# Optimization experiments

Measured on AMD Instinct MI355X. Metric: run time of the kernel, lower is better.

Reference implementation:

```python
import jax, jax.numpy as jnp
import numpy as np

N, D, NC, K = 4096, 64, 1000, 8192
ALPHA, BETA, GAMMA, SUPT = 0.02, 1.0, 1.0, 1.0
TEMP, BASE_TEMP = 0.05, 0.05
L_INTRA, L_IMEAN, L_IMIN, L_FISHER, EPS = 1.0, 0.1, 0.05, 0.1, 1e-6


def _l2norm(x, axis):
    # torch F.normalize: x / max(||x||, 1e-12)
    n = jnp.sqrt(jnp.sum(x * x, axis=axis, keepdims=True))
    return x / jnp.maximum(n, 1e-12)


def setup_inputs() -> dict:
    key = jax.random.key(0)
    k1, k2, k3, k4, k5 = jax.random.split(key, 5)
    # long-tailed class counts -> log_prior and class_weight buffers
    cls_arr = np.maximum((1280.0 * 0.01 ** (np.arange(NC) / (NC - 1))).astype(np.float32), 1.0)
    prior = cls_arr / cls_arr.sum()
    log_prior = jnp.asarray(np.log(prior), dtype=jnp.float32)
    inv = 1.0 / cls_arr
    class_weight = jnp.asarray((inv / inv.sum() * NC).astype(np.float32))
    feats = jax.random.normal(k1, (N, D), jnp.float32)
    logits = jax.random.normal(k2, (N, NC), jnp.float32)
    labels = jax.random.randint(k3, (N,), 0, NC)
    C = jax.random.normal(k4, (D, NC), jnp.float32) * 0.01  # learnable centers
    queue = jax.random.normal(k5, (K, D), jnp.float32)       # momentum queue buffer
    return {"feats": feats, "logits": logits, "labels": labels, "C": C,
            "queue": queue, "log_prior": log_prior, "class_weight": class_weight}


def reference(feats, logits, labels, C, queue, log_prior, class_weight):
    sg = jax.lax.stop_gradient
    # ---- weighted cross entropy on prior-adjusted logits ----
    sup_logits = (logits + log_prior) / SUPT
    logp = jax.nn.log_softmax(sup_logits, axis=1)
    w = class_weight[labels]
    nll = -jnp.take_along_axis(logp, labels[:, None], axis=1)[:, 0]
    ce_loss = jnp.sum(w * nll) / jnp.sum(w)

    # ---- normalize feats, enqueue (ptr=0, N<=K -> queue[:N] = feats) ----
    f = _l2norm(feats, axis=1)                       # [N, D]
    q = queue.at[:N].set(sg(f))                      # updated queue [K, D]
    centers = _l2norm(C, axis=0).T                   # [NC, D]

    neg_center_sim = f @ centers.T                   # [N, NC]
    neg_queue_sim = f @ q.T                          # [N, K]
    anchor_dot = jnp.concatenate([sg(sup_logits), neg_center_sim, neg_queue_sim], axis=1) / TEMP

    onehot = jax.nn.one_hot(labels, NC, dtype=jnp.float32)  # mask_sup == mask_cent
    mask = jnp.concatenate([onehot * BETA, onehot * ALPHA, jnp.zeros((N, K), jnp.float32)], axis=1)
    logits_mask = jnp.concatenate([jnp.ones((N, 2 * NC), jnp.float32),
                                   jnp.full((N, K), GAMMA, jnp.float32)], axis=1)

    anchor_dot = anchor_dot - sg(jnp.max(anchor_dot, axis=1, keepdims=True))
    exp_logits = jnp.exp(anchor_dot) * logits_mask
    log_prob = anchor_dot - jnp.log(jnp.sum(exp_logits, axis=1, keepdims=True) + 1e-12)
    mean_log_prob_pos = jnp.sum(mask * log_prob, axis=1) / (jnp.sum(mask, axis=1) + 1e-12)
    contrast_loss = -jnp.mean(mean_log_prob_pos) * (TEMP / BASE_TEMP)

    # ---- center regularizers ----
    gram = centers @ centers.T                       # centers are unit-norm rows
    sq = jnp.maximum(2.0 - 2.0 * gram, 1e-12)
    eye = jnp.eye(NC, dtype=bool)
    dist = jnp.sqrt(jnp.where(eye, 1e12, sq))
    dist_no_dg = jnp.where(eye, 1e6, dist)
    inter_min = jnp.min(dist_no_dg)
    inter_mean = jnp.sum(jnp.where(eye, 0.0, dist)) / (NC * (NC - 1))

    diff = f - centers[labels]                       # [N, D]
    intra_d = jnp.mean(jnp.sum(diff * diff, axis=1))
    mu_g = jnp.mean(f, axis=0, keepdims=True)
    cls_cnt = jnp.zeros((NC,), jnp.float32).at[labels].add(1.0)
    S_W = jnp.sum(diff * diff)
    S_B = jnp.sum(jnp.sum((centers - mu_g) ** 2, axis=1) * cls_cnt)
    fisher = S_B / (S_W + EPS)
    reg = (L_INTRA * intra_d + L_IMEAN / (inter_mean + EPS)
           + L_IMIN / (inter_min + EPS) + L_FISHER / (fisher + EPS))
    return ce_loss + contrast_loss + reg
```

## Files before the change

### kernel.cpp

```cpp
#include <hip/hip_runtime.h>
#include <math.h>

#define N_ 4096
#define D_ 64
#define NC_ 1000
#define KQ_ 8192
#define VCOLS 9192
#define VPAD  9216
#define PCH   5
#define TEMP_INV 20.0f
#define M0 20.25f
#define LOG2E 1.4426950408889634f
#define K2L  (TEMP_INV * LOG2E)
#define M0L  (M0 * LOG2E)

#define WS_F     0
#define WS_CENT  (WS_F + N_*D_)
#define WS_SUPM  (WS_CENT + NC_*D_)
#define WS_PSUP  (WS_SUPM + N_)
#define WS_PCENT (WS_PSUP + N_)
#define WS_CEPN  (WS_PCENT + N_)
#define WS_CEPD  (WS_CEPN + 1024)
#define WS_CSP   (WS_CEPD + 1024)
#define WS_GS    (WS_CSP + 16)
#define WS_GM    (WS_GS + 128)
#define WS_VF    (WS_GM + 128)
#define WS_VC    (WS_VF + 4096)
#define WS_TP    (WS_VC + 4096)
#define WS_CTR   (WS_TP + 64)
#define WS_PS    (WS_CTR + 4)
#define WS_BBF   (WS_PS + N_*PCH)

#define K1_BLOCKS 2058
#define K2_BLOCKS 1472
#define K3_BLOCKS 16

typedef __attribute__((ext_vector_type(8))) short short8_t;
typedef __attribute__((ext_vector_type(4))) float f32x4;

__device__ __forceinline__ ushort f2bf(float x) {
    union { float f; unsigned u; } v; v.f = x;
    unsigned r = (v.u + 0x7FFFu + ((v.u >> 16) & 1u)) >> 16;
    return (ushort)r;
}

__device__ __forceinline__ int swz(int byte) {
    return byte ^ (((byte >> 7) & 7) << 4);
}

__device__ __forceinline__ void gload16(const void* g, void* lds) {
    __builtin_amdgcn_global_load_lds(
        (const __attribute__((address_space(1))) unsigned int*)g,
        (__attribute__((address_space(3))) unsigned int*)lds, 16, 0, 0);
}

__global__ __launch_bounds__(256) void k1(const float* __restrict__ feats,
                                          const float* __restrict__ C,
                                          const float* __restrict__ queue,
                                          float* __restrict__ ws,
                                          ushort* __restrict__ B) {
    int b = blockIdx.x;
    int t = threadIdx.x;
    if (b == 0 && t == 0) ((unsigned*)ws)[WS_CTR] = 0u;
    if (b < 1024) {
        int row  = b * 4 + (t >> 6);
        int lane = t & 63;
        float x = feats[row * D_ + lane];
        float ss = x * x;
        #pragma unroll
        for (int m = 32; m >= 1; m >>= 1) ss += __shfl_xor(ss, m, 64);
        float y = x / fmaxf(sqrtf(ss), 1e-12f);
        ws[WS_F + row * D_ + lane] = y;
        B[(size_t)(NC_ + row) * D_ + lane] = f2bf(y);
    } else if (b < 1028) {
        int c = (b - 1024) * 256 + t;
        if (c >= NC_) return;
        float v[D_];
        float ss = 0.0f;
        #pragma unroll
        for (int d = 0; d < D_; ++d) { float x = C[d * NC_ + c]; v[d] = x; ss += x * x; }
        float inv = 1.0f / fmaxf(sqrtf(ss), 1e-12f);
        #pragma unroll
        for (int d = 0; d < D_; ++d) {
            float y = v[d] * inv;
            ws[WS_CENT + c * D_ + d] = y;
            B[(size_t)c * D_ + d] = f2bf(y);
        }
    } else {
        int q = (b - 1028) * 256 + t;
        if (q >= (KQ_ - N_ + 24) * D_) return;
        int r = q >> 6, d = q & 63;
        ushort o = 0;
        if (r < KQ_ - N_) o = f2bf(queue[(size_t)(N_ + r) * D_ + d]);
        B[(size_t)(NC_ + N_ + r) * D_ + d] = o;
    }
}

__global__ __launch_bounds__(256) void k2(const ushort* __restrict__ B,
                                          const float* __restrict__ logits,
                                          const int* __restrict__ labels,
                                          const float* __restrict__ log_prior,
                                          const float* __restrict__ class_weight,
                                          const float* __restrict__ f,
                                          const float* __restrict__ cent,
                                          float* __restrict__ ws) {
    __shared__ char smem[33280];
    int t = threadIdx.x;
    int l = t & 63, w = t >> 6;
    int bid = blockIdx.x;
    int wm = w >> 1, wn = w & 1;
    int lr = l & 15, lg = l >> 4;
    int lk = lg * 8;

    if (bid < 256) {
        char* buf0 = smem;
        char* buf1 = smem + 16384;
        float (*ssum)[2] = (float(*)[2])(smem + 32768);

        int bx = bid & 63, cg = bid >> 6;
        int r0 = bx * 64;
        int cbase = cg * 2304;

        const char* Ag = (const char*)(B + (size_t)(NC_ + r0) * D_);
        #pragma unroll
        for (int j = 0; j < 2; ++j) {
            int seg = w * 2 + j;
            int o = seg * 64 + l;
            int sc = o ^ ((o >> 3) & 7);
            gload16(Ag + sc * 16, buf0 + seg * 1024);
        }
        __syncthreads();
        short8_t a[2][2];
        #pragma unroll
        for (int rf = 0; rf < 2; ++rf) {
            int row = wm * 32 + rf * 16 + lr;
            #pragma unroll
            for (int ks = 0; ks < 2; ++ks)
                a[rf][ks] = *(const short8_t*)(buf0 + swz(row * 128 + ks * 64 + lg * 16));
        }
        __syncthreads();

        int lab[2][4];
        if (cg == 0) {
            #pragma unroll
            for (int rf = 0; rf < 2; ++rf)
                #pragma unroll
                for (int reg = 0; reg < 4; ++reg)
                    lab[rf][reg] = labels[r0 + wm * 32 + rf * 16 + lg * 4 + reg];
        }

        const char* Bg = (const char*)(B + (size_t)cbase * D_);
        auto stageB = [&](int tile, char* buf) {
            const char* Bt = Bg + (size_t)tile * 16384;
            #pragma unroll
            for (int j = 0; j < 4; ++j) {
                int seg = w * 4 + j;
                int o = seg * 64 + l;
                int sc = o ^ ((o >> 3) & 7);
                gload16(Bt + sc * 16, buf + seg * 1024);
            }
        };

        stageB(0, buf0);
        __syncthreads();

        float se[2][4] = {};
        #pragma unroll 2
        for (int it = 0; it < 18; ++it) {
            char* cur = (it & 1) ? buf1 : buf0;
            char* nxt = (it & 1) ? buf0 : buf1;
            if (it < 17) stageB(it + 1, nxt);

            short8_t bfr[4][2];
            #pragma unroll
            for (int cf = 0; cf < 4; ++cf) {
                int col = wn * 64 + cf * 16 + lr;
                #pragma unroll
                for (int ks = 0; ks < 2; ++ks)
                    bfr[cf][ks] = *(const short8_t*)(cur + swz(col * 128 + ks * 64 + lg * 16));
            }

            f32x4 acc[2][4] = {};
            #pragma unroll
            for (int ks = 0; ks < 2; ++ks)
                #pragma unroll
                for (int rf = 0; rf < 2; ++rf)
                    #pragma unroll
                    for (int cf = 0; cf < 4; ++cf)
                        acc[rf][cf] = __builtin_amdgcn_mfma_f32_16x16x32_bf16(
                            a[rf][ks], bfr[cf][ks], acc[rf][cf], 0, 0, 0);

            if (cg == 0 && it < 8) {
                #pragma unroll
                for (int rf = 0; rf < 2; ++rf)
                    #pragma unroll
                    for (int reg = 0; reg < 4; ++reg) {
                        #pragma unroll
                        for (int cf = 0; cf < 4; ++cf) {
                            int col = it * 128 + wn * 64 + cf * 16 + lr;
                            if (col == lab[rf][reg])
                                ws[WS_PCENT + r0 + wm * 32 + rf * 16 + lg * 4 + reg] =
                                    acc[rf][cf][reg];
                        }
                    }
            }

            #pragma unroll
            for (int rf = 0; rf < 2; ++rf)
                #pragma unroll
                for (int cf = 0; cf < 4; ++cf)
                    #pragma unroll
                    for (int reg = 0; reg < 4; ++reg)
                        se[rf][reg] += __builtin_amdgcn_exp2f(
                            fmaf(acc[rf][cf][reg], K2L, -M0L));

            __syncthreads();
        }

        #pragma unroll
        for (int rf = 0; rf < 2; ++rf)
            #pragma unroll
            for (int reg = 0; reg < 4; ++reg) {
                float v = se[rf][reg];
                #pragma unroll
                for (int msk = 1; msk < 16; msk <<= 1)
                    v += __shfl_xor(v, msk, 64);
                if (lr == 0) ssum[wm * 32 + rf * 16 + lg * 4 + reg][wn] = v;
            }
        __syncthreads();
        if (t < 64)
            ws[WS_PS + (size_t)(r0 + t) * PCH + cg] = ssum[t][0] + ssum[t][1];
    } else if (bid < 1280) {
        float* lp = (float*)smem;
        float (*cep)[2] = (float(*)[2])(smem + 4096);
        int sid = bid - 256;
        if (t < 250) ((float4*)lp)[t] = ((const float4*)log_prior)[t];
        __syncthreads();
        int row = sid * 4 + w;
        const float* lrow = logits + (size_t)row * NC_;
        const float4* lrow4 = (const float4*)lrow;
        float vals[16];
        float m = -1e30f;
        #pragma unroll
        for (int it = 0; it < 4; ++it) {
            int idx = it * 64 + l;
            float4 v4 = (idx < 250) ? lrow4[idx]
                                    : make_float4(-1e30f, -1e30f, -1e30f, -1e30f);
            float4 p4 = (idx < 250) ? ((const float4*)lp)[idx]
                                    : make_float4(0, 0, 0, 0);
            vals[it * 4 + 0] = v4.x + p4.x;
            vals[it * 4 + 1] = v4.y + p4.y;
            vals[it * 4 + 2] = v4.z + p4.z;
            vals[it * 4 + 3] = v4.w + p4.w;
            #pragma unroll
            for (int k = 0; k < 4; ++k) m = fmaxf(m, vals[it * 4 + k]);
        }
        #pragma unroll
        for (int msk = 1; msk < 64; msk <<= 1) m = fmaxf(m, __shfl_xor(m, msk, 64));
        float s1 = 0.0f, s20 = 0.0f;
        #pragma unroll
        for (int k = 0; k < 16; ++k) {
            float d = vals[k] - m;
            s1  += __builtin_amdgcn_exp2f(d * LOG2E);
            s20 += __builtin_amdgcn_exp2f(d * K2L);
        }
        #pragma unroll
        for (int msk = 1; msk < 64; msk <<= 1) {
            s1  += __shfl_xor(s1, msk, 64);
            s20 += __shfl_xor(s20, msk, 64);
        }
        if (l == 0) {
            int lab = labels[row];
            float vpos = lrow[lab] + lp[lab];
            float wt = class_weight[lab];
            cep[w][0] = wt * (m + __logf(s1) - vpos);
            cep[w][1] = wt;
            ws[WS_SUPM + row] = TEMP_INV * m;
            ws[WS_PS + (size_t)row * PCH + (PCH - 1)] = s20;
            ws[WS_PSUP + row] = TEMP_INV * vpos;
        }
        __syncthreads();
        if (t == 0) {
            ws[WS_CEPN + sid] = cep[0][0] + cep[1][0] + cep[2][0] + cep[3][0];
            ws[WS_CEPD + sid] = cep[0][1] + cep[1][1] + cep[2][1] + cep[3][1];
        }
    } else if (bid < 1408) {
        float* gs4 = (float*)smem;
        float* gm4 = gs4 + 4;
        int g = bid - 1280;
        int gr = g >> 3, gc = g & 7;
        int r0 = gr * 64 + wm * 32;
        int c0 = gc * 128 + wn * 64;

        const ushort* Af = B + (size_t)(r0 + lr) * D_ + lk;
        const ushort* Bf = B + (size_t)(c0 + lr) * D_ + lk;

        short8_t a[2][2], bfr[4][2];
        #pragma unroll
        for (int rf = 0; rf < 2; ++rf)
            #pragma unroll
            for (int ks = 0; ks < 2; ++ks)
                a[rf][ks] = *(const short8_t*)(Af + rf * 16 * D_ + ks * 32);
        #pragma unroll
        for (int cf = 0; cf < 4; ++cf)
            #pragma unroll
            for (int ks = 0; ks < 2; ++ks)
                bfr[cf][ks] = *(const short8_t*)(Bf + cf * 16 * D_ + ks * 32);

        f32x4 acc[2][4] = {};
        #pragma unroll
        for (int ks = 0; ks < 2; ++ks)
            #pragma unroll
            for (int rf = 0; rf < 2; ++rf)
                #pragma unroll
                for (int cf = 0; cf < 4; ++cf)
                    acc[rf][cf] = __builtin_amdgcn_mfma_f32_16x16x32_bf16(
                        a[rf][ks], bfr[cf][ks], acc[rf][cf], 0, 0, 0);

        float lsum = 0.0f, lmin = 1e30f;
        #pragma unroll
        for (int rf = 0; rf < 2; ++rf)
            #pragma unroll
            for (int cf = 0; cf < 4; ++cf)
                #pragma unroll
                for (int reg = 0; reg < 4; ++reg) {
                    int gi = r0 + rf * 16 + lg * 4 + reg;
                    int gj = c0 + cf * 16 + lr;
                    if (gi < NC_ && gj < NC_ && gi != gj) {
                        float d = sqrtf(fmaxf(2.0f - 2.0f * acc[rf][cf][reg], 1e-12f));
                        lsum += d;
                        lmin = fminf(lmin, d);
                    }
                }
        #pragma unroll
        for (int msk = 1; msk < 64; msk <<= 1) {
            lsum += __shfl_xor(lsum, msk, 64);
            lmin = fminf(lmin, __shfl_xor(lmin, msk, 64));
        }
        if (l == 0) { gs4[w] = lsum; gm4[w] = lmin; }
        __syncthreads();
        if (t == 0) {
            ws[WS_GS + g] = gs4[0] + gs4[1] + gs4[2] + gs4[3];
            ws[WS_GM + g] = fminf(fminf(gm4[0], gm4[1]), fminf(gm4[2], gm4[3]));
        }
    } else {
        float* svf = (float*)smem;
        float* svc = svf + 256;
        float* stp = svc + 256;
        int sb = bid - 1408;
        int wid = sb * 4 + w;
        float vf = 0.0f, vc = 0.0f, tacc = 0.0f;
        for (int i = wid; i < N_; i += 256) {
            float x = f[i * D_ + l];
            float c = cent[labels[i] * D_ + l];
            vf += x; vc += c; tacc += x * c;
        }
        #pragma unroll
        for (int msk = 32; msk >= 1; msk >>= 1) tacc += __shfl_xor(tacc, msk, 64);
        svf[w * 64 + l] = vf; svc[w * 64 + l] = vc;
        if (l == 0) stp[w] = tacc;
        __syncthreads();
        if (w == 0) {
            ws[WS_VF + sb * 64 + l] = svf[l] + svf[64 + l] + svf[128 + l] + svf[192 + l];
            ws[WS_VC + sb * 64 + l] = svc[l] + svc[64 + l] + svc[128 + l] + svc[192 + l];
            if (l == 0) ws[WS_TP + sb] = stp[0] + stp[1] + stp[2] + stp[3];
        }
    }
}

__global__ __launch_bounds__(256) void k3(float* __restrict__ ws,
                                          float* __restrict__ out) {
    int t = threadIdx.x;
    int w = t >> 6, l = t & 63;
    int bid = blockIdx.x;
    __shared__ unsigned done;
    __shared__ float cb[4];

    {
        int row = bid * 256 + t;
        const float* pv = ws + WS_PS + (size_t)row * PCH;
        float s = (pv[0] + pv[1]) + (pv[2] + pv[3]);
        float msup = ws[WS_SUPM + row];
        float ssup = pv[PCH - 1];
        float M = fmaxf(M0, msup);
        float stot = s * __builtin_amdgcn_exp2f((M0 - M) * LOG2E)
                   + ssup * __builtin_amdgcn_exp2f((msup - M) * LOG2E);
        float logS = __logf(stot + 1e-12f);
        float lp1 = ws[WS_PSUP + row] - M - logS;
        float lp2 = ws[WS_PCENT + row] * TEMP_INV - M - logS;
        float cacc = (lp1 + 0.02f * lp2) / (1.02f + 1e-12f);
        #pragma unroll
        for (int msk = 1; msk < 64; msk <<= 1) cacc += __shfl_xor(cacc, msk, 64);
        if (l == 0) cb[w] = cacc;
        __syncthreads();
        if (t == 0) ws[WS_CSP + bid] = cb[0] + cb[1] + cb[2] + cb[3];
    }

    __threadfence();
    if (t == 0) done = atomicAdd((unsigned*)ws + WS_CTR, 1u);
    __syncthreads();
    if (done != K3_BLOCKS - 1) return;
    __threadfence();

    float csum = (t < 16) ? ws[WS_CSP + t] : 0.0f;
    float cen = 0.0f, ced = 0.0f;
    #pragma unroll
    for (int k = 0; k < 4; ++k) {
        cen += ws[WS_CEPN + t + k * 256];
        ced += ws[WS_CEPD + t + k * 256];
    }
    float gsum = 0, gmin = 1e30f, vf = 0, vc = 0, tp = 0;
    if (t < 64) {
        tp = ws[WS_TP + t];
        #pragma unroll 8
        for (int b = 0; b < 64; ++b) {
            vf += ws[WS_VF + b * 64 + t];
            vc += ws[WS_VC + b * 64 + t];
        }
    }
    if (t < 128) { gsum = ws[WS_GS + t]; gmin = ws[WS_GM + t]; }
    float mu_d = vf * (1.0f / (float)N_);
    float vmu  = vc * mu_d;
    float mumu = mu_d * mu_d;
    #pragma unroll
    for (int m = 32; m >= 1; m >>= 1) {
        csum += __shfl_xor(csum, m, 64);
        cen  += __shfl_xor(cen, m, 64);
        ced  += __shfl_xor(ced, m, 64);
        gsum += __shfl_xor(gsum, m, 64);
        gmin = fminf(gmin, __shfl_xor(gmin, m, 64));
        vmu  += __shfl_xor(vmu, m, 64);
        mumu += __shfl_xor(mumu, m, 64);
        tp   += __shfl_xor(tp, m, 64);
    }
    __shared__ float red[4][8];
    if (l == 0) {
        red[w][0] = csum; red[w][1] = cen; red[w][2] = ced; red[w][3] = gsum;
        red[w][4] = gmin; red[w][5] = vmu; red[w][6] = mumu; red[w][7] = tp;
    }
    __syncthreads();
    if (t == 0) {
        float CSM = red[0][0] + red[1][0] + red[2][0] + red[3][0];
        float CEN = red[0][1] + red[1][1] + red[2][1] + red[3][1];
        float CED = red[0][2] + red[1][2] + red[2][2] + red[3][2];
        float GSM = red[0][3] + red[1][3] + red[2][3] + red[3][3];
        float GMN = fminf(fminf(red[0][4], red[1][4]), fminf(red[2][4], red[3][4]));
        float VMU = red[0][5] + red[1][5] + red[2][5] + red[3][5];
        float MUMU = red[0][6] + red[1][6] + red[2][6] + red[3][6];
        float T   = red[0][7] + red[1][7] + red[2][7] + red[3][7];
        float SW = 2.0f * (float)N_ - 2.0f * T;
        float SB = (float)N_ - 2.0f * VMU + (float)N_ * MUMU;
        float intra = SW / (float)N_;
        float fisher = SB / (SW + 1e-6f);
        float ce = CEN / CED;
        float contrast = -(CSM / (float)N_);
        float inter_mean = GSM / (float)(NC_ * (NC_ - 1));
        float reg = intra + 0.1f / (inter_mean + 1e-6f)
                  + 0.05f / (GMN + 1e-6f) + 0.1f / (fisher + 1e-6f);
        out[0] = ce + contrast + reg;
    }
}

extern "C" void kernel_launch(void* const* d_in, const int* in_sizes, int n_in,
                              void* d_out, int out_size, void* d_ws, size_t ws_size,
                              hipStream_t stream) {
    const float* feats        = (const float*)d_in[0];
    const float* logits       = (const float*)d_in[1];
    const int*   labels       = (const int*)d_in[2];
    const float* C            = (const float*)d_in[3];
    const float* queue        = (const float*)d_in[4];
    const float* log_prior    = (const float*)d_in[5];
    const float* class_weight = (const float*)d_in[6];
    float* ws  = (float*)d_ws;
    float* out = (float*)d_out;
    ushort* Bbf = (ushort*)(ws + WS_BBF);

    hipLaunchKernelGGL(k1, dim3(K1_BLOCKS), dim3(256), 0, stream,
                       feats, C, queue, ws, Bbf);
    hipLaunchKernelGGL(k2, dim3(K2_BLOCKS), dim3(256), 0, stream,
                       Bbf, logits, labels, log_prior, class_weight,
                       ws + WS_F, ws + WS_CENT, ws);
    hipLaunchKernelGGL(k3, dim3(K3_BLOCKS), dim3(256), 0, stream, ws, out);
}
```

Baseline: 41.50 us.

## Move CE pass into k1, split GEMM columns finer, fold final reduction into k2

```diff
diff --git a/kernel.cpp b/kernel.cpp
--- a/kernel.cpp
+++ b/kernel.cpp
@@ -7,7 +7,7 @@
 #define KQ_ 8192
 #define VCOLS 9192
 #define VPAD  9216
-#define PCH   5
+#define PCH   9
 #define TEMP_INV 20.0f
 #define M0 20.25f
 #define LOG2E 1.4426950408889634f
@@ -21,8 +21,7 @@
 #define WS_PCENT (WS_PSUP + N_)
 #define WS_CEPN  (WS_PCENT + N_)
 #define WS_CEPD  (WS_CEPN + 1024)
-#define WS_CSP   (WS_CEPD + 1024)
-#define WS_GS    (WS_CSP + 16)
+#define WS_GS    (WS_CEPD + 1024)
 #define WS_GM    (WS_GS + 128)
 #define WS_VF    (WS_GM + 128)
 #define WS_VC    (WS_VF + 4096)
@@ -31,9 +30,8 @@
 #define WS_PS    (WS_CTR + 4)
 #define WS_BBF   (WS_PS + N_*PCH)
 
-#define K1_BLOCKS 2058
-#define K2_BLOCKS 1472
-#define K3_BLOCKS 16
+#define K1_BLOCKS 3082
+#define K2_BLOCKS 704
 
 typedef __attribute__((ext_vector_type(8))) short short8_t;
 typedef __attribute__((ext_vector_type(4))) float f32x4;
@@ -57,8 +55,14 @@
 __global__ __launch_bounds__(256) void k1(const float* __restrict__ feats,
                                           const float* __restrict__ C,
                                           const float* __restrict__ queue,
+                                          const float* __restrict__ logits,
+                                          const int* __restrict__ labels,
+                                          const float* __restrict__ log_prior,
+                                          const float* __restrict__ class_weight,
                                           float* __restrict__ ws,
                                           ushort* __restrict__ B) {
+    __shared__ float lp[1024];
+    __shared__ float cep[4][2];
     int b = blockIdx.x;
     int t = threadIdx.x;
     if (b == 0 && t == 0) ((unsigned*)ws)[WS_CTR] = 0u;
@@ -86,24 +90,75 @@
             ws[WS_CENT + c * D_ + d] = y;
             B[(size_t)c * D_ + d] = f2bf(y);
         }
-    } else {
+    } else if (b < 2058) {
         int q = (b - 1028) * 256 + t;
         if (q >= (KQ_ - N_ + 24) * D_) return;
         int r = q >> 6, d = q & 63;
         ushort o = 0;
         if (r < KQ_ - N_) o = f2bf(queue[(size_t)(N_ + r) * D_ + d]);
         B[(size_t)(NC_ + N_ + r) * D_ + d] = o;
+    } else {
+        int sid = b - 2058;
+        if (t < 250) ((float4*)lp)[t] = ((const float4*)log_prior)[t];
+        __syncthreads();
+        int w = t >> 6, l = t & 63;
+        int row = sid * 4 + w;
+        const float* lrow = logits + (size_t)row * NC_;
+        const float4* lrow4 = (const float4*)lrow;
+        float vals[16];
+        float m = -1e30f;
+        #pragma unroll
+        for (int it = 0; it < 4; ++it) {
+            int idx = it * 64 + l;
+            float4 v4 = (idx < 250) ? lrow4[idx]
+                                    : make_float4(-1e30f, -1e30f, -1e30f, -1e30f);
+            float4 p4 = (idx < 250) ? ((const float4*)lp)[idx]
+                                    : make_float4(0, 0, 0, 0);
+            vals[it * 4 + 0] = v4.x + p4.x;
+            vals[it * 4 + 1] = v4.y + p4.y;
+            vals[it * 4 + 2] = v4.z + p4.z;
+            vals[it * 4 + 3] = v4.w + p4.w;
+            #pragma unroll
+            for (int k = 0; k < 4; ++k) m = fmaxf(m, vals[it * 4 + k]);
+        }
+        #pragma unroll
+        for (int msk = 1; msk < 64; msk <<= 1) m = fmaxf(m, __shfl_xor(m, msk, 64));
+        float s1 = 0.0f, s20 = 0.0f;
+        #pragma unroll
+        for (int k = 0; k < 16; ++k) {
+            float d = vals[k] - m;
+            s1  += __builtin_amdgcn_exp2f(d * LOG2E);
+            s20 += __builtin_amdgcn_exp2f(d * K2L);
+        }
+        #pragma unroll
+        for (int msk = 1; msk < 64; msk <<= 1) {
+            s1  += __shfl_xor(s1, msk, 64);
+            s20 += __shfl_xor(s20, msk, 64);
+        }
+        if (l == 0) {
+            int lab = labels[row];
+            float vpos = lrow[lab] + lp[lab];
+            float wt = class_weight[lab];
+            cep[w][0] = wt * (m + __logf(s1) - vpos);
+            cep[w][1] = wt;
+            ws[WS_SUPM + row] = TEMP_INV * m;
+            ws[WS_PS + (size_t)row * PCH + (PCH - 1)] = s20;
+            ws[WS_PSUP + row] = TEMP_INV * vpos;
+        }
+        __syncthreads();
+        if (t == 0) {
+            ws[WS_CEPN + sid] = cep[0][0] + cep[1][0] + cep[2][0] + cep[3][0];
+            ws[WS_CEPD + sid] = cep[0][1] + cep[1][1] + cep[2][1] + cep[3][1];
+        }
     }
 }
 
 __global__ __launch_bounds__(256) void k2(const ushort* __restrict__ B,
-                                          const float* __restrict__ logits,
                                           const int* __restrict__ labels,
-                                          const float* __restrict__ log_prior,
-                                          const float* __restrict__ class_weight,
                                           const float* __restrict__ f,
                                           const float* __restrict__ cent,
-                                          float* __restrict__ ws) {
+                                          float* __restrict__ ws,
+                                          float* __restrict__ out) {
     __shared__ char smem[33280];
     int t = threadIdx.x;
     int l = t & 63, w = t >> 6;
@@ -112,14 +167,14 @@
     int lr = l & 15, lg = l >> 4;
     int lk = lg * 8;
 
-    if (bid < 256) {
+    if (bid < 512) {
         char* buf0 = smem;
         char* buf1 = smem + 16384;
         float (*ssum)[2] = (float(*)[2])(smem + 32768);
 
         int bx = bid & 63, cg = bid >> 6;
         int r0 = bx * 64;
-        int cbase = cg * 2304;
+        int cbase = cg * 1152;
 
         const char* Ag = (const char*)(B + (size_t)(NC_ + r0) * D_);
         #pragma unroll
@@ -165,11 +220,11 @@
         __syncthreads();
 
         float se[2][4] = {};
-        #pragma unroll 2
-        for (int it = 0; it < 18; ++it) {
+        #pragma unroll 3
+        for (int it = 0; it < 9; ++it) {
             char* cur = (it & 1) ? buf1 : buf0;
             char* nxt = (it & 1) ? buf0 : buf1;
-            if (it < 17) stageB(it + 1, nxt);
+            if (it < 8) stageB(it + 1, nxt);
 
             short8_t bfr[4][2];
             #pragma unroll
@@ -230,64 +285,10 @@
         __syncthreads();
         if (t < 64)
             ws[WS_PS + (size_t)(r0 + t) * PCH + cg] = ssum[t][0] + ssum[t][1];
-    } else if (bid < 1280) {
-        float* lp = (float*)smem;
-        float (*cep)[2] = (float(*)[2])(smem + 4096);
-        int sid = bid - 256;
-        if (t < 250) ((float4*)lp)[t] = ((const float4*)log_prior)[t];
-        __syncthreads();
-        int row = sid * 4 + w;
-        const float* lrow = logits + (size_t)row * NC_;
-        const float4* lrow4 = (const float4*)lrow;
-        float vals[16];
-        float m = -1e30f;
-        #pragma unroll
-        for (int it = 0; it < 4; ++it) {
-            int idx = it * 64 + l;
-            float4 v4 = (idx < 250) ? lrow4[idx]
-                                    : make_float4(-1e30f, -1e30f, -1e30f, -1e30f);
-            float4 p4 = (idx < 250) ? ((const float4*)lp)[idx]
-                                    : make_float4(0, 0, 0, 0);
-            vals[it * 4 + 0] = v4.x + p4.x;
-            vals[it * 4 + 1] = v4.y + p4.y;
-            vals[it * 4 + 2] = v4.z + p4.z;
-            vals[it * 4 + 3] = v4.w + p4.w;
-            #pragma unroll
-            for (int k = 0; k < 4; ++k) m = fmaxf(m, vals[it * 4 + k]);
-        }
-        #pragma unroll
-        for (int msk = 1; msk < 64; msk <<= 1) m = fmaxf(m, __shfl_xor(m, msk, 64));
-        float s1 = 0.0f, s20 = 0.0f;
-        #pragma unroll
-        for (int k = 0; k < 16; ++k) {
-            float d = vals[k] - m;
-            s1  += __builtin_amdgcn_exp2f(d * LOG2E);
-            s20 += __builtin_amdgcn_exp2f(d * K2L);
-        }
-        #pragma unroll
-        for (int msk = 1; msk < 64; msk <<= 1) {
-            s1  += __shfl_xor(s1, msk, 64);
-            s20 += __shfl_xor(s20, msk, 64);
-        }
-        if (l == 0) {
-            int lab = labels[row];
-            float vpos = lrow[lab] + lp[lab];
-            float wt = class_weight[lab];
-            cep[w][0] = wt * (m + __logf(s1) - vpos);
-            cep[w][1] = wt;
-            ws[WS_SUPM + row] = TEMP_INV * m;
-            ws[WS_PS + (size_t)row * PCH + (PCH - 1)] = s20;
-            ws[WS_PSUP + row] = TEMP_INV * vpos;
-        }
-        __syncthreads();
-        if (t == 0) {
-            ws[WS_CEPN + sid] = cep[0][0] + cep[1][0] + cep[2][0] + cep[3][0];
-            ws[WS_CEPD + sid] = cep[0][1] + cep[1][1] + cep[2][1] + cep[3][1];
-        }
-    } else if (bid < 1408) {
+    } else if (bid < 640) {
         float* gs4 = (float*)smem;
         float* gm4 = gs4 + 4;
-        int g = bid - 1280;
+        int g = bid - 512;
         int gr = g >> 3, gc = g & 7;
         int r0 = gr * 64 + wm * 32;
         int c0 = gc * 128 + wn * 64;
@@ -347,7 +348,7 @@
         float* svf = (float*)smem;
         float* svc = svf + 256;
         float* stp = svc + 256;
-        int sb = bid - 1408;
+        int sb = bid - 640;
         int wid = sb * 4 + w;
         float vf = 0.0f, vc = 0.0f, tacc = 0.0f;
         for (int i = wid; i < N_; i += 256) {
@@ -366,20 +367,22 @@
             if (l == 0) ws[WS_TP + sb] = stp[0] + stp[1] + stp[2] + stp[3];
         }
     }
-}
-
-__global__ __launch_bounds__(256) void k3(float* __restrict__ ws,
-                                          float* __restrict__ out) {
-    int t = threadIdx.x;
-    int w = t >> 6, l = t & 63;
-    int bid = blockIdx.x;
+
     __shared__ unsigned done;
-    __shared__ float cb[4];
-
-    {
-        int row = bid * 256 + t;
+    __threadfence();
+    __syncthreads();
+    if (t == 0) done = atomicAdd((unsigned*)ws + WS_CTR, 1u);
+    __syncthreads();
+    if (done != K2_BLOCKS - 1) return;
+    __threadfence();
+
+    float cacc = 0.0f;
+    for (int q = 0; q < 16; ++q) {
+        int row = q * 256 + t;
         const float* pv = ws + WS_PS + (size_t)row * PCH;
-        float s = (pv[0] + pv[1]) + (pv[2] + pv[3]);
+        float s = 0.0f;
+        #pragma unroll
+        for (int c = 0; c < PCH - 1; ++c) s += pv[c];
         float msup = ws[WS_SUPM + row];
         float ssup = pv[PCH - 1];
         float M = fmaxf(M0, msup);
@@ -388,21 +391,8 @@
         float logS = __logf(stot + 1e-12f);
         float lp1 = ws[WS_PSUP + row] - M - logS;
         float lp2 = ws[WS_PCENT + row] * TEMP_INV - M - logS;
-        float cacc = (lp1 + 0.02f * lp2) / (1.02f + 1e-12f);
-        #pragma unroll
-        for (int msk = 1; msk < 64; msk <<= 1) cacc += __shfl_xor(cacc, msk, 64);
-        if (l == 0) cb[w] = cacc;
-        __syncthreads();
-        if (t == 0) ws[WS_CSP + bid] = cb[0] + cb[1] + cb[2] + cb[3];
-    }
-
-    __threadfence();
-    if (t == 0) done = atomicAdd((unsigned*)ws + WS_CTR, 1u);
-    __syncthreads();
-    if (done != K3_BLOCKS - 1) return;
-    __threadfence();
-
-    float csum = (t < 16) ? ws[WS_CSP + t] : 0.0f;
+        cacc += (lp1 + 0.02f * lp2) / (1.02f + 1e-12f);
+    }
     float cen = 0.0f, ced = 0.0f;
     #pragma unroll
     for (int k = 0; k < 4; ++k) {
@@ -424,7 +414,7 @@
     float mumu = mu_d * mu_d;
     #pragma unroll
     for (int m = 32; m >= 1; m >>= 1) {
-        csum += __shfl_xor(csum, m, 64);
+        cacc += __shfl_xor(cacc, m, 64);
         cen  += __shfl_xor(cen, m, 64);
         ced  += __shfl_xor(ced, m, 64);
         gsum += __shfl_xor(gsum, m, 64);
@@ -433,21 +423,22 @@
         mumu += __shfl_xor(mumu, m, 64);
         tp   += __shfl_xor(tp, m, 64);
     }
-    __shared__ float red[4][8];
+    float* red = (float*)smem;
     if (l == 0) {
-        red[w][0] = csum; red[w][1] = cen; red[w][2] = ced; red[w][3] = gsum;
-        red[w][4] = gmin; red[w][5] = vmu; red[w][6] = mumu; red[w][7] = tp;
+        red[w * 8 + 0] = cacc; red[w * 8 + 1] = cen; red[w * 8 + 2] = ced;
+        red[w * 8 + 3] = gsum; red[w * 8 + 4] = gmin; red[w * 8 + 5] = vmu;
+        red[w * 8 + 6] = mumu; red[w * 8 + 7] = tp;
     }
     __syncthreads();
     if (t == 0) {
-        float CSM = red[0][0] + red[1][0] + red[2][0] + red[3][0];
-        float CEN = red[0][1] + red[1][1] + red[2][1] + red[3][1];
-        float CED = red[0][2] + red[1][2] + red[2][2] + red[3][2];
-        float GSM = red[0][3] + red[1][3] + red[2][3] + red[3][3];
-        float GMN = fminf(fminf(red[0][4], red[1][4]), fminf(red[2][4], red[3][4]));
-        float VMU = red[0][5] + red[1][5] + red[2][5] + red[3][5];
-        float MUMU = red[0][6] + red[1][6] + red[2][6] + red[3][6];
-        float T   = red[0][7] + red[1][7] + red[2][7] + red[3][7];
+        float CSM = red[0] + red[8] + red[16] + red[24];
+        float CEN = red[1] + red[9] + red[17] + red[25];
+        float CED = red[2] + red[10] + red[18] + red[26];
+        float GSM = red[3] + red[11] + red[19] + red[27];
+        float GMN = fminf(fminf(red[4], red[12]), fminf(red[20], red[28]));
+        float VMU = red[5] + red[13] + red[21] + red[29];
+        float MUMU = red[6] + red[14] + red[22] + red[30];
+        float T   = red[7] + red[15] + red[23] + red[31];
         float SW = 2.0f * (float)N_ - 2.0f * T;
         float SB = (float)N_ - 2.0f * VMU + (float)N_ * MUMU;
         float intra = SW / (float)N_;
@@ -476,9 +467,8 @@
     ushort* Bbf = (ushort*)(ws + WS_BBF);
 
     hipLaunchKernelGGL(k1, dim3(K1_BLOCKS), dim3(256), 0, stream,
-                       feats, C, queue, ws, Bbf);
+                       feats, C, queue, logits, labels, log_prior, class_weight,
+                       ws, Bbf);
     hipLaunchKernelGGL(k2, dim3(K2_BLOCKS), dim3(256), 0, stream,
-                       Bbf, logits, labels, log_prior, class_weight,
-                       ws + WS_F, ws + WS_CENT, ws);
-    hipLaunchKernelGGL(k3, dim3(K3_BLOCKS), dim3(256), 0, stream, ws, out);
-}
+                       Bbf, labels, ws + WS_F, ws + WS_CENT, ws, out);
+}
```

Result: slower. 89.23 us (+115.0%).
